# Kernel optimization log

Measured on AMD Instinct MI355X. Metric: run time of the kernel, lower is better.

The kernel has to match this reference:

```python
import jax, jax.numpy as jnp
import numpy as np

B, T, C, U, W = 8, 2048, 512, 512, 2


def setup_inputs() -> dict:
    key = jax.random.key(0)
    k1, k2 = jax.random.split(key)
    x = jax.random.normal(k1, (B, T, C), dtype=jnp.float32)
    # Conv1D kernel: [window, in_channels, 3*units] (z, f, o gates), glorot-ish scale
    kernel = jax.random.normal(k2, (W, C, 3 * U), dtype=jnp.float32) * (1.0 / np.sqrt(W * C))
    bias = jnp.zeros((3 * U,), dtype=jnp.float32)
    initial_state = jnp.zeros((1, U), dtype=jnp.float32)
    return {"x": x, "kernel": kernel, "bias": bias, "initial_state": initial_state}


def reference(x, kernel, bias, initial_state):
    # Causal Conv1D: pad (window-1) on the left of the time axis.
    window = kernel.shape[0]
    gates = jax.lax.conv_general_dilated(
        x, kernel,
        window_strides=(1,),
        padding=[(window - 1, 0)],
        dimension_numbers=("NWC", "WIO", "NWC"),
    ) + bias  # [B, T, 3U]
    z, f, o = jnp.split(gates, 3, axis=-1)
    z = jnp.tanh(z)
    f = jax.nn.sigmoid(f)
    o = jax.nn.sigmoid(o)

    # fo-pool recurrence: h_t = f_t * h_{t-1} + (1 - f_t) * z_t
    h0 = jnp.repeat(initial_state, x.shape[0], axis=0)  # [B, U]
    fs = jnp.moveaxis(f, 1, 0)  # [T, B, U]
    zs = jnp.moveaxis(z, 1, 0)  # [T, B, U]

    def step(h, fz):
        f_t, z_t = fz
        h = f_t * h + (1.0 - f_t) * z_t
        return h, h

    _, hs = jax.lax.scan(step, h0, (fs, zs))  # hs: [T, B, U]
    recurrent = jnp.moveaxis(hs, 0, 1)  # [B, T, U]

    # output gate, return_sequences=True
    return recurrent * o
```

## Files before the change

### kernel.cpp

```cpp
#include <hip/hip_runtime.h>


#define Bn 8
#define Tn 2048
#define Cn 512
#define Un 512
#define Nn 1536
#define Kn 1024
#define Mn (Bn * Tn)
#define NC 32
#define CL 64

using bf16x8 = __attribute__((ext_vector_type(8))) __bf16;
using f32x4  = __attribute__((ext_vector_type(4))) float;

__device__ __forceinline__ void async16(const void* g, void* l) {
  __builtin_amdgcn_global_load_lds((const __attribute__((address_space(1))) void*)g,
                                   (__attribute__((address_space(3))) void*)l, 16, 0, 0);
}

__device__ __forceinline__ unsigned short f2bf(float v) {
  union { float f; unsigned u; } c; c.f = v;
  unsigned u = c.u;
  return (unsigned short)((u + 0x7fffu + ((u >> 16) & 1u)) >> 16);
}

__device__ __forceinline__ float fast_sigmoid(float x) {
  float e = __builtin_amdgcn_exp2f(-1.4426950408889634f * x);
  return __builtin_amdgcn_rcpf(1.0f + e);
}
__device__ __forceinline__ float fast_tanh(float x) {
  float e = __builtin_amdgcn_exp2f(-2.8853900817779268f * x);
  return 2.0f * __builtin_amdgcn_rcpf(1.0f + e) - 1.0f;
}

__global__ __launch_bounds__(256) void conv_x(const float* __restrict__ x,
                                              unsigned short* __restrict__ xb) {
  int idx = blockIdx.x * 256 + threadIdx.x;
  int c4  = idx & 127;
  int row = idx >> 7;
  int b   = row / (Tn + 1);
  int t   = row - b * (Tn + 1);
  ushort4 ov;
  if (t == 0) {
    ov.x = ov.y = ov.z = ov.w = 0;
  } else {
    float4 v = *(const float4*)(x + (size_t)(b * Tn + t - 1) * Cn + c4 * 4);
    ov.x = f2bf(v.x); ov.y = f2bf(v.y); ov.z = f2bf(v.z); ov.w = f2bf(v.w);
  }
  *(ushort4*)(xb + (size_t)row * Cn + c4 * 4) = ov;
}

__global__ __launch_bounds__(256) void conv_k(const float* __restrict__ kern,
                                              unsigned short* __restrict__ kT) {
  __shared__ float tile[32][33];
  int kb = blockIdx.x, nb = blockIdx.y;
  int tx = threadIdx.x & 31, ty = threadIdx.x >> 5;
#pragma unroll
  for (int i = 0; i < 4; i++)
    tile[ty + i * 8][tx] = kern[(size_t)(kb * 32 + ty + i * 8) * Nn + nb * 32 + tx];
  __syncthreads();
#pragma unroll
  for (int i = 0; i < 4; i++) {
    int n = nb * 32 + ty + i * 8;
    int k = kb * 32 + tx;
    kT[(size_t)n * Kn + k] = f2bf(tile[tx][ty + i * 8]);
  }
}

__global__ __launch_bounds__(256) void gemm_gates(const unsigned short* __restrict__ xb,
                                                  const unsigned short* __restrict__ kT,
                                                  const float* __restrict__ bias,
                                                  float* __restrict__ gates) {
  __shared__ unsigned short As[128 * 32];
  __shared__ unsigned short Bs[128 * 32];
  const int tid = threadIdx.x;
  const int m0 = blockIdx.x * 128;
  const int n0 = blockIdx.y * 128;
  const int batch = m0 / Tn;
  const int lane = tid & 63;
  const int w = tid >> 6, wr = w >> 1, wc = w & 1;

  const unsigned short* aSrc = xb + (size_t)(m0 + batch + (tid >> 2)) * Cn + (tid & 3) * 8;
  const unsigned short* bSrc = kT + (size_t)(n0 + (tid >> 2)) * Kn + (tid & 3) * 8;

  f32x4 zero = {0.f, 0.f, 0.f, 0.f};
  f32x4 acc[4][4];
#pragma unroll
  for (int i = 0; i < 4; i++)
#pragma unroll
    for (int j = 0; j < 4; j++) acc[i][j] = zero;

  for (int k0 = 0; k0 < Kn; k0 += 32) {
    async16(aSrc + k0,            &As[tid * 8]);
    async16(aSrc + 64 * Cn + k0,  &As[2048 + tid * 8]);
    async16(bSrc + k0,            &Bs[tid * 8]);
    async16(bSrc + 64 * Kn + k0,  &Bs[2048 + tid * 8]);
    __builtin_amdgcn_s_waitcnt(0);
    __syncthreads();

    const int kq = (lane >> 4) * 8;
    const int rA = wr * 64 + (lane & 15);
    const int rB = wc * 64 + (lane & 15);
    bf16x8 af[4], bf[4];
#pragma unroll
    for (int i = 0; i < 4; i++) af[i] = *(const bf16x8*)&As[(rA + i * 16) * 32 + kq];
#pragma unroll
    for (int j = 0; j < 4; j++) bf[j] = *(const bf16x8*)&Bs[(rB + j * 16) * 32 + kq];
#pragma unroll
    for (int i = 0; i < 4; i++)
#pragma unroll
      for (int j = 0; j < 4; j++)
        acc[i][j] = __builtin_amdgcn_mfma_f32_16x16x32_bf16(af[i], bf[j], acc[i][j], 0, 0, 0);
    __syncthreads();
  }

  const int region = blockIdx.y >> 2;
  const int rowB = wr * 64 + (lane >> 4) * 4;
  const int colB = wc * 64 + (lane & 15);
#pragma unroll
  for (int i = 0; i < 4; i++)
#pragma unroll
    for (int j = 0; j < 4; j++)
#pragma unroll
      for (int r = 0; r < 4; r++) {
        int mm = m0 + rowB + i * 16 + r;
        int nn = n0 + colB + j * 16;
        float g = acc[i][j][r] + bias[nn];
        float a = (region == 0) ? fast_tanh(g) : fast_sigmoid(g);
        gates[(size_t)mm * Nn + nn] = a;
      }
}

__global__ __launch_bounds__(512) void scan_phaseA(const float* __restrict__ gates,
                                                   float* __restrict__ aArr,
                                                   float* __restrict__ bArr) {
  int u = threadIdx.x;
  int blk = blockIdx.x;
  int b = blk >> 5, c = blk & (NC - 1);
  const float* gp = gates + (size_t)(b * Tn + c * CL) * Nn;
  float a = 1.0f, bv = 0.0f;
#pragma unroll 4
  for (int t = 0; t < CL; t++) {
    float z = gp[u];
    float f = gp[Un + u];
    a *= f;
    bv = f * bv + (1.0f - f) * z;
    gp += Nn;
  }
  aArr[(size_t)blk * Un + u] = a;
  bArr[(size_t)blk * Un + u] = bv;
}

__global__ __launch_bounds__(256) void scan_phaseB(const float* __restrict__ aArr,
                                                   const float* __restrict__ bArr,
                                                   const float* __restrict__ init,
                                                   float* __restrict__ hstart) {
  int idx = blockIdx.x * 256 + threadIdx.x;
  int b = idx >> 9, u = idx & (Un - 1);
  float h = init[u];
  for (int c = 0; c < NC; c++) {
    size_t offc = (size_t)(b * NC + c) * Un + u;
    hstart[offc] = h;
    h = aArr[offc] * h + bArr[offc];
  }
}

__global__ __launch_bounds__(512) void scan_phaseC(const float* __restrict__ gates,
                                                   const float* __restrict__ hstart,
                                                   float* __restrict__ out) {
  int u = threadIdx.x;
  int blk = blockIdx.x;
  int b = blk >> 5, c = blk & (NC - 1);
  const float* gp = gates + (size_t)(b * Tn + c * CL) * Nn;
  float* op = out + (size_t)(b * Tn + c * CL) * Un;
  float h = hstart[(size_t)blk * Un + u];
#pragma unroll 4
  for (int t = 0; t < CL; t++) {
    float z = gp[u];
    float f = gp[Un + u];
    float o = gp[2 * Un + u];
    h = f * h + (1.0f - f) * z;
    op[u] = h * o;
    gp += Nn;
    op += Un;
  }
}

extern "C" void kernel_launch(void* const* d_in, const int* in_sizes, int n_in,
                              void* d_out, int out_size, void* d_ws, size_t ws_size,
                              hipStream_t stream) {
  const float* x    = (const float*)d_in[0];
  const float* kern = (const float*)d_in[1];
  const float* bias = (const float*)d_in[2];
  const float* init = (const float*)d_in[3];
  float* out = (float*)d_out;

  char* ws = (char*)d_ws;
  unsigned short* xb = (unsigned short*)ws;
  size_t off = (size_t)Bn * (Tn + 1) * Cn * 2;
  unsigned short* kT = (unsigned short*)(ws + off);
  off += (size_t)Nn * Kn * 2;
  float* gates = (float*)(ws + off);
  off += (size_t)Mn * Nn * 4;
  float* aArr = (float*)(ws + off);  off += (size_t)Bn * NC * Un * 4;
  float* bArr = (float*)(ws + off);  off += (size_t)Bn * NC * Un * 4;
  float* hstart = (float*)(ws + off);

  conv_x<<<(Bn * (Tn + 1) * Cn / 4) / 256, 256, 0, stream>>>(x, xb);
  conv_k<<<dim3(32, 48), 256, 0, stream>>>(kern, kT);
  gemm_gates<<<dim3(Mn / 128, Nn / 128), 256, 0, stream>>>(xb, kT, bias, gates);
  scan_phaseA<<<Bn * NC, 512, 0, stream>>>(gates, aArr, bArr);
  scan_phaseB<<<(Bn * Un) / 256, 256, 0, stream>>>(aArr, bArr, init, hstart);
  scan_phaseC<<<Bn * NC, 512, 0, stream>>>(gates, hstart, out);
}
```

Measured before the change: 188.1 us.

## Double-buffer B tile in LDS, stream A to registers, shorten scan chunks

The gates GEMM no longer stages A through shared memory. Each wave loads its A fragments straight from global memory into registers, one k-step ahead. The B tile is double-buffered in LDS in a k-major layout, so the next tile's async load overlaps the current MFMAs and one barrier per iteration is removed. The chunked scan now uses 64 chunks of 32 steps instead of 32 of 64, with a larger unroll, to expose more parallelism in phases A and C. The risks are less coalesced, uncached-in-LDS A loads that rely on L1/L2 for reuse, and a longer sequential phase B.

New measurement: 266.7 us. +41.8%, slower.

```diff
diff --git a/kernel.cpp b/kernel.cpp
--- a/kernel.cpp
+++ b/kernel.cpp
@@ -8,8 +8,8 @@
 #define Nn 1536
 #define Kn 1024
 #define Mn (Bn * Tn)
-#define NC 32
-#define CL 64
+#define NC 64
+#define CL 32
 
 using bf16x8 = __attribute__((ext_vector_type(8))) __bf16;
 using f32x4  = __attribute__((ext_vector_type(4))) float;
@@ -72,8 +72,7 @@
                                                   const unsigned short* __restrict__ kT,
                                                   const float* __restrict__ bias,
                                                   float* __restrict__ gates) {
-  __shared__ unsigned short As[128 * 32];
-  __shared__ unsigned short Bs[128 * 32];
+  __shared__ unsigned short Bs[2][4096];
   const int tid = threadIdx.x;
   const int m0 = blockIdx.x * 128;
   const int n0 = blockIdx.y * 128;
@@ -81,8 +80,11 @@
   const int lane = tid & 63;
   const int w = tid >> 6, wr = w >> 1, wc = w & 1;
 
-  const unsigned short* aSrc = xb + (size_t)(m0 + batch + (tid >> 2)) * Cn + (tid & 3) * 8;
-  const unsigned short* bSrc = kT + (size_t)(n0 + (tid >> 2)) * Kn + (tid & 3) * 8;
+  const unsigned short* bRow = kT + (size_t)(n0 + (tid & 127)) * Kn + (tid >> 7) * 8;
+
+  const unsigned short* aBase = xb + (size_t)(m0 + batch + wr * 64 + (lane & 15)) * Cn
+                                   + (lane >> 4) * 8;
+  const int bOff = (lane >> 4) * 1024 + (wc * 64 + (lane & 15)) * 8;
 
   f32x4 zero = {0.f, 0.f, 0.f, 0.f};
   f32x4 acc[4][4];
@@ -91,28 +93,32 @@
 #pragma unroll
     for (int j = 0; j < 4; j++) acc[i][j] = zero;
 
+  async16(bRow, &Bs[0][tid * 8]);
+  async16(bRow + 16, &Bs[0][2048 + tid * 8]);
+  bf16x8 afc[4], afn[4];
+#pragma unroll
+  for (int i = 0; i < 4; i++) afc[i] = *(const bf16x8*)(aBase + (size_t)i * 16 * Cn);
+
   for (int k0 = 0; k0 < Kn; k0 += 32) {
-    async16(aSrc + k0,            &As[tid * 8]);
-    async16(aSrc + 64 * Cn + k0,  &As[2048 + tid * 8]);
-    async16(bSrc + k0,            &Bs[tid * 8]);
-    async16(bSrc + 64 * Kn + k0,  &Bs[2048 + tid * 8]);
-    __builtin_amdgcn_s_waitcnt(0);
+    const int buf = (k0 >> 5) & 1;
     __syncthreads();
-
-    const int kq = (lane >> 4) * 8;
-    const int rA = wr * 64 + (lane & 15);
-    const int rB = wc * 64 + (lane & 15);
-    bf16x8 af[4], bf[4];
-#pragma unroll
-    for (int i = 0; i < 4; i++) af[i] = *(const bf16x8*)&As[(rA + i * 16) * 32 + kq];
-#pragma unroll
-    for (int j = 0; j < 4; j++) bf[j] = *(const bf16x8*)&Bs[(rB + j * 16) * 32 + kq];
+    if (k0 + 32 < Kn) {
+      async16(bRow + k0 + 32, &Bs[buf ^ 1][tid * 8]);
+      async16(bRow + k0 + 48, &Bs[buf ^ 1][2048 + tid * 8]);
+#pragma unroll
+      for (int i = 0; i < 4; i++)
+        afn[i] = *(const bf16x8*)(aBase + (size_t)i * 16 * Cn + k0 + 32);
+    }
+    bf16x8 bfr[4];
+#pragma unroll
+    for (int j = 0; j < 4; j++) bfr[j] = *(const bf16x8*)&Bs[buf][bOff + j * 16 * 8];
 #pragma unroll
     for (int i = 0; i < 4; i++)
 #pragma unroll
       for (int j = 0; j < 4; j++)
-        acc[i][j] = __builtin_amdgcn_mfma_f32_16x16x32_bf16(af[i], bf[j], acc[i][j], 0, 0, 0);
-    __syncthreads();
+        acc[i][j] = __builtin_amdgcn_mfma_f32_16x16x32_bf16(afc[i], bfr[j], acc[i][j], 0, 0, 0);
+#pragma unroll
+    for (int i = 0; i < 4; i++) afc[i] = afn[i];
   }
 
   const int region = blockIdx.y >> 2;
@@ -137,10 +143,10 @@
                                                    float* __restrict__ bArr) {
   int u = threadIdx.x;
   int blk = blockIdx.x;
-  int b = blk >> 5, c = blk & (NC - 1);
+  int b = blk >> 6, c = blk & (NC - 1);
   const float* gp = gates + (size_t)(b * Tn + c * CL) * Nn;
   float a = 1.0f, bv = 0.0f;
-#pragma unroll 4
+#pragma unroll 8
   for (int t = 0; t < CL; t++) {
     float z = gp[u];
     float f = gp[Un + u];
@@ -171,11 +177,11 @@
                                                    float* __restrict__ out) {
   int u = threadIdx.x;
   int blk = blockIdx.x;
-  int b = blk >> 5, c = blk & (NC - 1);
+  int b = blk >> 6, c = blk & (NC - 1);
   const float* gp = gates + (size_t)(b * Tn + c * CL) * Nn;
   float* op = out + (size_t)(b * Tn + c * CL) * Un;
   float h = hstart[(size_t)blk * Un + u];
-#pragma unroll 4
+#pragma unroll 8
   for (int t = 0; t < CL; t++) {
     float z = gp[u];
     float f = gp[Un + u];
```
